# Kernel tuning notes

Hardware: AMD Instinct MI355X
Metric: run time of the kernel (lower is better)

## Reference

```python
import jax, jax.numpy as jnp
import numpy as np

S = 100000   # unique_source_num
T = 20000    # unique_target_num
N = S + T    # total nodes (sources first, then targets)
E = 1000000  # edges
SRC_DIM, EMB_DIM, TGT_DIM = 256, 128, 128


def setup_inputs() -> dict:
    key = jax.random.key(0)
    ks = jax.random.split(key, 6)
    source_feat = jax.random.normal(ks[0], (N, SRC_DIM), dtype=jnp.float32)
    src_idx = jax.random.randint(ks[1], (E,), 0, S)            # edge sources in [0, S)
    dst_idx = jax.random.randint(ks[2], (E,), 0, T)            # edge targets, target-local in [0, T)
    range_list = jax.random.randint(ks[3], (T, 2), 0, S)       # unused by the math (passed through in torch)
    # x_norm divides features; keep it bounded away from 0 like real row norms
    x_norm = jax.random.uniform(ks[4], (N,), dtype=jnp.float32, minval=0.5, maxval=1.5)
    k_e, k_w = jax.random.split(ks[5])
    embed = jax.random.normal(k_e, (SRC_DIM, EMB_DIM), dtype=jnp.float32)          # Param, std=1 init
    weight = jax.random.normal(k_w, (EMB_DIM, TGT_DIM), dtype=jnp.float32) / np.sqrt(EMB_DIM)  # is_after_relu std=1/sqrt(in)
    return {"source_feat": source_feat, "src_idx": src_idx, "dst_idx": dst_idx,
            "range_list": range_list, "x_norm": x_norm, "embed": embed, "weight": weight}


def reference(source_feat, src_idx, dst_idx, range_list, x_norm, embed, weight):
    # x = (source_feat @ embed) / x_norm[:, None]   -> [N, EMB_DIM]
    x = jnp.matmul(source_feat, embed) / x_norm[:, None]
    # message + scatter-mean aggregation onto targets (sources receive no edges,
    # so aggregating directly over the T targets == aggr_out[S:] in the torch code)
    msgs = x[src_idx]                                           # [E, EMB_DIM] gather
    summed = jax.ops.segment_sum(msgs, dst_idx, num_segments=T) # [T, EMB_DIM]
    cnt = jax.ops.segment_sum(jnp.ones((E,), dtype=x.dtype), dst_idx, num_segments=T)
    aggr = summed / jnp.maximum(cnt, 1.0)[:, None]              # mean; zero-degree -> 0
    out = jnp.matmul(aggr, weight)                              # [T, TGT_DIM]
    return out
```

## Files before the change

kernel.cpp:

```cpp
#include <hip/hip_runtime.h>
#include <cstdint>
#include <cstddef>

#define S_NUM 100000
#define T_NUM 20000
#define E_NUM 1000000

#define NB   1250
#define GT   16
#define CAP  1280
#define CH   4096
#define KB2  245
#define KB1  1563

typedef __bf16 bf16x8 __attribute__((ext_vector_type(8)));
typedef float f32x4 __attribute__((ext_vector_type(4)));

__device__ __forceinline__ unsigned short f2bf(float f) {
  unsigned int u = __float_as_uint(f);
  u += 0x7fffu + ((u >> 16) & 1u);
  return (unsigned short)(u >> 16);
}
__device__ __forceinline__ unsigned int f2bf2(float lo, float hi) {
  return (unsigned int)f2bf(lo) | ((unsigned int)f2bf(hi) << 16);
}
__device__ __forceinline__ float bflo(unsigned int v) { return __uint_as_float(v << 16); }
__device__ __forceinline__ float bfhi(unsigned int v) { return __uint_as_float(v & 0xffff0000u); }

__launch_bounds__(512)
__global__ void k12_fused(const float* __restrict__ sf, const float* __restrict__ xn,
                          const float* __restrict__ embed, unsigned short* __restrict__ xb,
                          const int* __restrict__ src_idx, const int* __restrict__ dst_idx,
                          int* __restrict__ gcursor, unsigned int* __restrict__ ebuf) {
  __shared__ __align__(16) unsigned char smem[64 * 296 * 2];
  const int tid = threadIdx.x;

  if (blockIdx.x < KB2) {
    int* bcnt  = (int*)smem;
    int* gbase = (int*)(smem + 5120);
    const int e0 = blockIdx.x * CH;
    const int e1 = (e0 + CH < E_NUM) ? (e0 + CH) : E_NUM;
    for (int i = tid; i < NB; i += 512) bcnt[i] = 0;
    __syncthreads();
    for (int e = e0 + tid; e < e1; e += 512)
      atomicAdd(&bcnt[dst_idx[e] >> 4], 1);
    __syncthreads();
    for (int i = tid; i < NB; i += 512) {
      const int cnt = bcnt[i];
      gbase[i] = (cnt > 0) ? atomicAdd(&gcursor[i], cnt) : 0;
      bcnt[i] = 0;
    }
    __syncthreads();
    for (int e = e0 + tid; e < e1; e += 512) {
      const int d = dst_idx[e];
      const int s = src_idx[e];
      const int b = d >> 4;
      const int r = atomicAdd(&bcnt[b], 1);
      const int pos = gbase[b] + r;
      if (pos < CAP)
        ebuf[(size_t)b * CAP + pos] = ((unsigned int)(d & 15) << 17) | (unsigned int)s;
    }
    return;
  }

  unsigned short (*lA)[296] = (unsigned short (*)[296])smem;
  unsigned short (*lC)[136] = (unsigned short (*)[136])smem;
  const int wave = tid >> 6;
  const int lane = tid & 63;
  const int quad = lane >> 4;
  const int l15 = lane & 15;
  const int row0 = (blockIdx.x - KB2) * 64;
  const int col0 = wave * 16;

  bf16x8 fb[8];
#pragma unroll
  for (int kc = 0; kc < 8; ++kc) {
    union { unsigned short h[8]; bf16x8 v; } u;
#pragma unroll
    for (int j = 0; j < 8; ++j)
      u.h[j] = f2bf(embed[(size_t)(kc * 32 + quad * 8 + j) * 128 + col0 + l15]);
    fb[kc] = u.v;
  }

#pragma unroll
  for (int i = 0; i < 4; ++i) {
    const int idx = i * 512 + tid;
    const int row = idx >> 5;
    const int seg = idx & 31;
    const float4* g = (const float4*)(sf + (size_t)(row0 + row) * 256 + seg * 8);
    const float4 v0 = g[0];
    const float4 v1 = g[1];
    uint4 pk;
    pk.x = f2bf2(v0.x, v0.y);
    pk.y = f2bf2(v0.z, v0.w);
    pk.z = f2bf2(v1.x, v1.y);
    pk.w = f2bf2(v1.z, v1.w);
    *(uint4*)&lA[row][seg * 8] = pk;
  }
  __syncthreads();

  f32x4 acc[4];
#pragma unroll
  for (int i = 0; i < 4; ++i) acc[i] = (f32x4){0.f, 0.f, 0.f, 0.f};

#pragma unroll
  for (int kc = 0; kc < 8; ++kc)
#pragma unroll
    for (int rt = 0; rt < 4; ++rt) {
      bf16x8 fa = *(const bf16x8*)&lA[rt * 16 + l15][kc * 32 + quad * 8];
      acc[rt] = __builtin_amdgcn_mfma_f32_16x16x32_bf16(fa, fb[kc], acc[rt], 0, 0, 0);
    }
  __syncthreads();

#pragma unroll
  for (int rt = 0; rt < 4; ++rt) {
#pragma unroll
    for (int reg = 0; reg < 4; ++reg) {
      const int row = rt * 16 + quad * 4 + reg;
      const float inv = __builtin_amdgcn_rcpf(xn[row0 + row]);
      lC[row][col0 + l15] = f2bf(acc[rt][reg] * inv);
    }
  }
  __syncthreads();

#pragma unroll
  for (int p = 0; p < 2; ++p) {
    const int i = p * 512 + tid;
    const int row = i >> 4;
    const int seg = i & 15;
    const int gr = row0 + row;
    if (gr < S_NUM)
      *(uint4*)(xb + (size_t)gr * 128 + seg * 8) = *(const uint4*)&lC[row][seg * 8];
  }
}

__launch_bounds__(512)
__global__ void k3_fused(const int* __restrict__ gcursor, const unsigned int* __restrict__ ebuf,
                         const unsigned short* __restrict__ xb,
                         const float* __restrict__ weight,
                         float* __restrict__ out) {
  __shared__ unsigned int sls[CAP];
  __shared__ int hist[GT], scn[GT], cur[GT];
  __shared__ unsigned int Pu[GT][68];
  const int b = blockIdx.x;
  const int tid = threadIdx.x;
  const int wave = tid >> 6, lane = tid & 63;
  const int quad = lane >> 4, l15 = lane & 15;

  int n = gcursor[b];
  if (n > CAP) n = CAP;
  const unsigned int* eb = ebuf + (size_t)b * CAP;

  if (tid < GT) hist[tid] = 0;
  __syncthreads();
  for (int i = tid; i < n; i += 512) atomicAdd(&hist[eb[i] >> 17], 1);
  __syncthreads();
  if (tid == 0) {
    int run = 0;
#pragma unroll
    for (int i = 0; i < GT; ++i) { scn[i] = run; run += hist[i]; }
  }
  __syncthreads();
  if (tid < GT) cur[tid] = scn[tid];
  __syncthreads();
  for (int i = tid; i < n; i += 512) {
    const unsigned int e = eb[i];
    const int r = atomicAdd(&cur[e >> 17], 1);
    sls[r] = e & 0x1FFFFu;
  }
  __syncthreads();

#pragma unroll
  for (int rep = 0; rep < 2; ++rep) {
    const int tl = wave * 2 + rep;
    const int beg = scn[tl];
    const int c = hist[tl];
    float a0 = 0.f, a1 = 0.f, b0 = 0.f, b1 = 0.f;
    int e = 0;
    for (; e + 16 <= c; e += 16) {
      int s[16];
#pragma unroll
      for (int j = 0; j < 16; ++j) s[j] = (int)sls[beg + e + j];
      unsigned int v[16];
#pragma unroll
      for (int j = 0; j < 16; ++j)
        v[j] = *(const unsigned int*)(xb + (size_t)s[j] * 128 + 2 * lane);
#pragma unroll
      for (int j = 0; j < 16; j += 2) {
        a0 += bflo(v[j]);     a1 += bfhi(v[j]);
        b0 += bflo(v[j + 1]); b1 += bfhi(v[j + 1]);
      }
    }
    for (; e + 4 <= c; e += 4) {
      int s[4];
#pragma unroll
      for (int j = 0; j < 4; ++j) s[j] = (int)sls[beg + e + j];
      unsigned int v[4];
#pragma unroll
      for (int j = 0; j < 4; ++j)
        v[j] = *(const unsigned int*)(xb + (size_t)s[j] * 128 + 2 * lane);
      a0 += bflo(v[0]); a1 += bfhi(v[0]);
      b0 += bflo(v[1]); b1 += bfhi(v[1]);
      a0 += bflo(v[2]); a1 += bfhi(v[2]);
      b0 += bflo(v[3]); b1 += bfhi(v[3]);
    }
    for (; e < c; ++e) {
      const int s0 = (int)sls[beg + e];
      const unsigned int v0 = *(const unsigned int*)(xb + (size_t)s0 * 128 + 2 * lane);
      a0 += bflo(v0); a1 += bfhi(v0);
    }
    a0 += b0; a1 += b1;
    const float inv = (c > 0) ? __builtin_amdgcn_rcpf((float)c) : 0.f;
    Pu[tl][lane] = f2bf2(a0 * inv, a1 * inv);
  }
  __syncthreads();

  const int ncol = wave * 16 + l15;
  bf16x8 wb[4];
#pragma unroll
  for (int kc = 0; kc < 4; ++kc) {
    union { unsigned short h[8]; bf16x8 v; } u;
#pragma unroll
    for (int j = 0; j < 8; ++j)
      u.h[j] = f2bf(weight[(size_t)(kc * 32 + quad * 8 + j) * 128 + ncol]);
    wb[kc] = u.v;
  }
  f32x4 o0 = (f32x4){0.f, 0.f, 0.f, 0.f};
#pragma unroll
  for (int kc = 0; kc < 4; ++kc) {
    bf16x8 p0 = *(const bf16x8*)((const unsigned short*)&Pu[l15][0] + kc * 32 + quad * 8);
    o0 = __builtin_amdgcn_mfma_f32_16x16x32_bf16(p0, wb[kc], o0, 0, 0, 0);
  }
#pragma unroll
  for (int reg = 0; reg < 4; ++reg)
    out[((size_t)b * GT + quad * 4 + reg) * 128 + ncol] = o0[reg];
}

extern "C" void kernel_launch(void* const* d_in, const int* in_sizes, int n_in,
                              void* d_out, int out_size, void* d_ws, size_t ws_size,
                              hipStream_t stream) {
  const float* sf      = (const float*)d_in[0];
  const int*   src_idx = (const int*)d_in[1];
  const int*   dst_idx = (const int*)d_in[2];
  const float* xn      = (const float*)d_in[4];
  const float* embed   = (const float*)d_in[5];
  const float* weight  = (const float*)d_in[6];
  float* out = (float*)d_out;

  char* w = (char*)d_ws;
  unsigned short* xb = (unsigned short*)(w);
  int* gcursor       = (int*)(w + 25600000);
  unsigned int* ebuf = (unsigned int*)(w + 25608192);

  hipMemsetAsync(gcursor, 0, 8192, stream);
  k12_fused<<<KB2 + KB1, 512, 0, stream>>>(sf, xn, embed, xb, src_idx, dst_idx, gcursor, ebuf);
  k3_fused<<<NB, 512, 0, stream>>>(gcursor, ebuf, xb, weight, out);
}
```

Measured before the change: 247.0 us.

## Pre-transpose weights to bf16 in prep kernel and widen gather loads

Adds a small prep kernel that zeroes the bucket cursors (replacing the memset) and writes bf16 transposed copies of embed and weight. The GEMM blocks then load their B fragments with single 16-byte vector loads instead of eight strided fp32 loads with per-element conversion. The gather loop is restructured so each half-wave handles alternate edges with 8-byte loads, and the halves are combined with a cross-lane shuffle. The cost is an extra kernel launch and a dependency on the prep kernel before the main work starts.

After: 247.1 us. Within noise of the previous version (+0.1%).

```diff
diff --git a/kernel.cpp b/kernel.cpp
--- a/kernel.cpp
+++ b/kernel.cpp
@@ -27,9 +27,27 @@
 __device__ __forceinline__ float bflo(unsigned int v) { return __uint_as_float(v << 16); }
 __device__ __forceinline__ float bfhi(unsigned int v) { return __uint_as_float(v & 0xffff0000u); }
 
+__launch_bounds__(256)
+__global__ void k0_prep(const float* __restrict__ embed, const float* __restrict__ weight,
+                        int* __restrict__ gcursor, unsigned short* __restrict__ embedT,
+                        unsigned short* __restrict__ weightT) {
+  const int idx = blockIdx.x * 256 + threadIdx.x;
+  if (idx < 2048) gcursor[idx] = 0;
+  {
+    const int col = idx & 127;
+    const int k = idx >> 7;
+    embedT[(size_t)col * 256 + k] = f2bf(embed[(size_t)k * 128 + col]);
+  }
+  if (idx < 16384) {
+    const int n = idx & 127;
+    const int k = idx >> 7;
+    weightT[(size_t)n * 128 + k] = f2bf(weight[(size_t)k * 128 + n]);
+  }
+}
+
 __launch_bounds__(512)
 __global__ void k12_fused(const float* __restrict__ sf, const float* __restrict__ xn,
-                          const float* __restrict__ embed, unsigned short* __restrict__ xb,
+                          const unsigned short* __restrict__ embedT, unsigned short* __restrict__ xb,
                           const int* __restrict__ src_idx, const int* __restrict__ dst_idx,
                           int* __restrict__ gcursor, unsigned int* __restrict__ ebuf) {
   __shared__ __align__(16) unsigned char smem[64 * 296 * 2];
@@ -72,15 +90,11 @@
   const int row0 = (blockIdx.x - KB2) * 64;
   const int col0 = wave * 16;
 
+  const unsigned short* ebT = embedT + (size_t)(col0 + l15) * 256;
   bf16x8 fb[8];
 #pragma unroll
-  for (int kc = 0; kc < 8; ++kc) {
-    union { unsigned short h[8]; bf16x8 v; } u;
-#pragma unroll
-    for (int j = 0; j < 8; ++j)
-      u.h[j] = f2bf(embed[(size_t)(kc * 32 + quad * 8 + j) * 128 + col0 + l15]);
-    fb[kc] = u.v;
-  }
+  for (int kc = 0; kc < 8; ++kc)
+    fb[kc] = *(const bf16x8*)(ebT + kc * 32 + quad * 8);
 
 #pragma unroll
   for (int i = 0; i < 4; ++i) {
@@ -137,7 +151,7 @@
 __launch_bounds__(512)
 __global__ void k3_fused(const int* __restrict__ gcursor, const unsigned int* __restrict__ ebuf,
                          const unsigned short* __restrict__ xb,
-                         const float* __restrict__ weight,
+                         const unsigned short* __restrict__ weightT,
                          float* __restrict__ out) {
   __shared__ unsigned int sls[CAP];
   __shared__ int hist[GT], scn[GT], cur[GT];
@@ -170,61 +184,57 @@
   }
   __syncthreads();
 
+  const int h = lane >> 5;
+  const int cq = lane & 31;
 #pragma unroll
   for (int rep = 0; rep < 2; ++rep) {
     const int tl = wave * 2 + rep;
     const int beg = scn[tl];
     const int c = hist[tl];
-    float a0 = 0.f, a1 = 0.f, b0 = 0.f, b1 = 0.f;
+    float t0 = 0.f, t1 = 0.f, t2 = 0.f, t3 = 0.f;
     int e = 0;
     for (; e + 16 <= c; e += 16) {
-      int s[16];
-#pragma unroll
-      for (int j = 0; j < 16; ++j) s[j] = (int)sls[beg + e + j];
-      unsigned int v[16];
-#pragma unroll
-      for (int j = 0; j < 16; ++j)
-        v[j] = *(const unsigned int*)(xb + (size_t)s[j] * 128 + 2 * lane);
-#pragma unroll
-      for (int j = 0; j < 16; j += 2) {
-        a0 += bflo(v[j]);     a1 += bfhi(v[j]);
-        b0 += bflo(v[j + 1]); b1 += bfhi(v[j + 1]);
+      int s[8];
+#pragma unroll
+      for (int j = 0; j < 8; ++j) s[j] = (int)sls[beg + e + 2 * j + h];
+      uint2 v[8];
+#pragma unroll
+      for (int j = 0; j < 8; ++j)
+        v[j] = *(const uint2*)(xb + (size_t)s[j] * 128 + 4 * cq);
+#pragma unroll
+      for (int j = 0; j < 8; ++j) {
+        t0 += bflo(v[j].x); t1 += bfhi(v[j].x);
+        t2 += bflo(v[j].y); t3 += bfhi(v[j].y);
       }
     }
-    for (; e + 4 <= c; e += 4) {
-      int s[4];
-#pragma unroll
-      for (int j = 0; j < 4; ++j) s[j] = (int)sls[beg + e + j];
-      unsigned int v[4];
-#pragma unroll
-      for (int j = 0; j < 4; ++j)
-        v[j] = *(const unsigned int*)(xb + (size_t)s[j] * 128 + 2 * lane);
-      a0 += bflo(v[0]); a1 += bfhi(v[0]);
-      b0 += bflo(v[1]); b1 += bfhi(v[1]);
-      a0 += bflo(v[2]); a1 += bfhi(v[2]);
-      b0 += bflo(v[3]); b1 += bfhi(v[3]);
-    }
-    for (; e < c; ++e) {
-      const int s0 = (int)sls[beg + e];
-      const unsigned int v0 = *(const unsigned int*)(xb + (size_t)s0 * 128 + 2 * lane);
-      a0 += bflo(v0); a1 += bfhi(v0);
-    }
-    a0 += b0; a1 += b1;
+    for (; e + 2 <= c; e += 2) {
+      const int s0 = (int)sls[beg + e + h];
+      const uint2 v0 = *(const uint2*)(xb + (size_t)s0 * 128 + 4 * cq);
+      t0 += bflo(v0.x); t1 += bfhi(v0.x);
+      t2 += bflo(v0.y); t3 += bfhi(v0.y);
+    }
+    if ((c & 1) && h == 0) {
+      const int s0 = (int)sls[beg + c - 1];
+      const uint2 v0 = *(const uint2*)(xb + (size_t)s0 * 128 + 4 * cq);
+      t0 += bflo(v0.x); t1 += bfhi(v0.x);
+      t2 += bflo(v0.y); t3 += bfhi(v0.y);
+    }
+    t0 += __shfl_xor(t0, 32, 64);
+    t1 += __shfl_xor(t1, 32, 64);
+    t2 += __shfl_xor(t2, 32, 64);
+    t3 += __shfl_xor(t3, 32, 64);
     const float inv = (c > 0) ? __builtin_amdgcn_rcpf((float)c) : 0.f;
-    Pu[tl][lane] = f2bf2(a0 * inv, a1 * inv);
+    const unsigned int pk = h ? f2bf2(t2 * inv, t3 * inv) : f2bf2(t0 * inv, t1 * inv);
+    Pu[tl][2 * cq + h] = pk;
   }
   __syncthreads();
 
   const int ncol = wave * 16 + l15;
+  const unsigned short* wT = weightT + (size_t)ncol * 128;
   bf16x8 wb[4];
 #pragma unroll
-  for (int kc = 0; kc < 4; ++kc) {
-    union { unsigned short h[8]; bf16x8 v; } u;
-#pragma unroll
-    for (int j = 0; j < 8; ++j)
-      u.h[j] = f2bf(weight[(size_t)(kc * 32 + quad * 8 + j) * 128 + ncol]);
-    wb[kc] = u.v;
-  }
+  for (int kc = 0; kc < 4; ++kc)
+    wb[kc] = *(const bf16x8*)(wT + kc * 32 + quad * 8);
   f32x4 o0 = (f32x4){0.f, 0.f, 0.f, 0.f};
 #pragma unroll
   for (int kc = 0; kc < 4; ++kc) {
@@ -248,11 +258,13 @@
   float* out = (float*)d_out;
 
   char* w = (char*)d_ws;
-  unsigned short* xb = (unsigned short*)(w);
-  int* gcursor       = (int*)(w + 25600000);
-  unsigned int* ebuf = (unsigned int*)(w + 25608192);
-
-  hipMemsetAsync(gcursor, 0, 8192, stream);
-  k12_fused<<<KB2 + KB1, 512, 0, stream>>>(sf, xn, embed, xb, src_idx, dst_idx, gcursor, ebuf);
-  k3_fused<<<NB, 512, 0, stream>>>(gcursor, ebuf, xb, weight, out);
-}
+  unsigned short* xb      = (unsigned short*)(w);
+  int* gcursor            = (int*)(w + 25600000);
+  unsigned int* ebuf      = (unsigned int*)(w + 25608192);
+  unsigned short* embedT  = (unsigned short*)(w + 32008192);
+  unsigned short* weightT = (unsigned short*)(w + 32073728);
+
+  k0_prep<<<128, 256, 0, stream>>>(embed, weight, gcursor, embedT, weightT);
+  k12_fused<<<KB2 + KB1, 512, 0, stream>>>(sf, xn, embedT, xb, src_idx, dst_idx, gcursor, ebuf);
+  k3_fused<<<NB, 512, 0, stream>>>(gcursor, ebuf, xb, weightT, out);
+}
```

## Replace global-atomic edge bucketing with per-chunk LDS sort and chunk-indexed gather

Applied to the files above, without the earlier changes.

Each edge chunk now sorts its edges by target bucket in LDS using a block-wide prefix scan. It writes the sorted chunk out contiguously, along with per-chunk bucket counts and offsets. The aggregation kernel rebuilds each bucket's edge list by scanning the per-chunk counts and binary-searching into the chunk array. This removes the global cursor atomics, the memset, and the scattered 4-byte writes into the bucket buffer. In exchange it adds strided count/base reads, an extra scan and binary search per bucket, and fragmented gather reads in the aggregation kernel.

Measured after the change: 241.1 us. 2.4% less time.

```diff
diff --git a/kernel.cpp b/kernel.cpp
--- a/kernel.cpp
+++ b/kernel.cpp
@@ -31,34 +31,74 @@
 __global__ void k12_fused(const float* __restrict__ sf, const float* __restrict__ xn,
                           const float* __restrict__ embed, unsigned short* __restrict__ xb,
                           const int* __restrict__ src_idx, const int* __restrict__ dst_idx,
-                          int* __restrict__ gcursor, unsigned int* __restrict__ ebuf) {
+                          unsigned int* __restrict__ echunk, int* __restrict__ counts,
+                          int* __restrict__ bases) {
   __shared__ __align__(16) unsigned char smem[64 * 296 * 2];
   const int tid = threadIdx.x;
 
   if (blockIdx.x < KB2) {
     int* bcnt  = (int*)smem;
-    int* gbase = (int*)(smem + 5120);
-    const int e0 = blockIdx.x * CH;
+    int* scan  = (int*)(smem + 5120);
+    int* brank = (int*)(smem + 10240);
+    unsigned int* eLDS = (unsigned int*)(smem + 15360);
+    const int c = blockIdx.x;
+    const int e0 = c * CH;
     const int e1 = (e0 + CH < E_NUM) ? (e0 + CH) : E_NUM;
-    for (int i = tid; i < NB; i += 512) bcnt[i] = 0;
-    __syncthreads();
-    for (int e = e0 + tid; e < e1; e += 512)
-      atomicAdd(&bcnt[dst_idx[e] >> 4], 1);
-    __syncthreads();
+
+    int myd[8], mys[8];
+#pragma unroll
+    for (int k = 0; k < 8; ++k) {
+      const int e = e0 + k * 512 + tid;
+      const bool ok = e < e1;
+      myd[k] = ok ? dst_idx[e] : -1;
+      mys[k] = ok ? src_idx[e] : 0;
+    }
+    for (int i = tid; i < 1280; i += 512) bcnt[i] = 0;
+    __syncthreads();
+#pragma unroll
+    for (int k = 0; k < 8; ++k)
+      if (myd[k] >= 0) atomicAdd(&bcnt[myd[k] >> 4], 1);
+    __syncthreads();
+    for (int i = tid; i < 1280; i += 512) scan[i] = bcnt[i];
+    __syncthreads();
+    for (int st = 1; st < 1280; st <<= 1) {
+      int v0 = 0, v1 = 0, v2 = 0;
+      {
+        const int j0 = tid, j1 = tid + 512, j2 = tid + 1024;
+        if (j0 >= st) v0 = scan[j0 - st];
+        if (j1 >= st) v1 = scan[j1 - st];
+        if (j2 < 1280 && j2 >= st) v2 = scan[j2 - st];
+      }
+      __syncthreads();
+      {
+        const int j0 = tid, j1 = tid + 512, j2 = tid + 1024;
+        scan[j0] += v0;
+        scan[j1] += v1;
+        if (j2 < 1280) scan[j2] += v2;
+      }
+      __syncthreads();
+    }
     for (int i = tid; i < NB; i += 512) {
       const int cnt = bcnt[i];
-      gbase[i] = (cnt > 0) ? atomicAdd(&gcursor[i], cnt) : 0;
-      bcnt[i] = 0;
-    }
-    __syncthreads();
-    for (int e = e0 + tid; e < e1; e += 512) {
-      const int d = dst_idx[e];
-      const int s = src_idx[e];
-      const int b = d >> 4;
-      const int r = atomicAdd(&bcnt[b], 1);
-      const int pos = gbase[b] + r;
-      if (pos < CAP)
-        ebuf[(size_t)b * CAP + pos] = ((unsigned int)(d & 15) << 17) | (unsigned int)s;
+      const int base = scan[i] - cnt;
+      counts[(size_t)c * NB + i] = cnt;
+      bases[(size_t)c * NB + i] = base;
+      brank[i] = base;
+    }
+    __syncthreads();
+#pragma unroll
+    for (int k = 0; k < 8; ++k)
+      if (myd[k] >= 0) {
+        const int b = myd[k] >> 4;
+        const int r = atomicAdd(&brank[b], 1);
+        eLDS[r] = ((unsigned int)(myd[k] & 15) << 17) | (unsigned int)mys[k];
+      }
+    __syncthreads();
+    {
+      uint4* dst = (uint4*)(echunk + (size_t)c * CH);
+      const uint4* src = (const uint4*)eLDS;
+      dst[tid] = src[tid];
+      dst[512 + tid] = src[512 + tid];
     }
     return;
   }
@@ -135,10 +175,13 @@
 }
 
 __launch_bounds__(512)
-__global__ void k3_fused(const int* __restrict__ gcursor, const unsigned int* __restrict__ ebuf,
+__global__ void k3_fused(const unsigned int* __restrict__ echunk, const int* __restrict__ counts,
+                         const int* __restrict__ bases,
                          const unsigned short* __restrict__ xb,
                          const float* __restrict__ weight,
                          float* __restrict__ out) {
+  __shared__ int ccnt[256], cpre[256], cbas[256];
+  __shared__ unsigned int tmp[CAP];
   __shared__ unsigned int sls[CAP];
   __shared__ int hist[GT], scn[GT], cur[GT];
   __shared__ unsigned int Pu[GT][68];
@@ -147,13 +190,39 @@
   const int wave = tid >> 6, lane = tid & 63;
   const int quad = lane >> 4, l15 = lane & 15;
 
-  int n = gcursor[b];
+  if (tid < 256) {
+    if (tid < KB2) {
+      ccnt[tid] = counts[(size_t)tid * NB + b];
+      cbas[tid] = bases[(size_t)tid * NB + b];
+    } else { ccnt[tid] = 0; cbas[tid] = 0; }
+  }
+  __syncthreads();
+  if (tid < 256) cpre[tid] = ccnt[tid];
+  __syncthreads();
+  for (int st = 1; st < 256; st <<= 1) {
+    int v = 0;
+    if (tid < 256 && tid >= st) v = cpre[tid - st];
+    __syncthreads();
+    if (tid < 256) cpre[tid] += v;
+    __syncthreads();
+  }
+  int n = cpre[255];
   if (n > CAP) n = CAP;
-  const unsigned int* eb = ebuf + (size_t)b * CAP;
+
+  for (int i = tid; i < n; i += 512) {
+    int lo = 0, hi = 255;
+    while (lo < hi) {
+      const int mid = (lo + hi) >> 1;
+      if (cpre[mid] > i) hi = mid; else lo = mid + 1;
+    }
+    const int off = i - (cpre[lo] - ccnt[lo]);
+    tmp[i] = echunk[(size_t)lo * CH + cbas[lo] + off];
+  }
+  __syncthreads();
 
   if (tid < GT) hist[tid] = 0;
   __syncthreads();
-  for (int i = tid; i < n; i += 512) atomicAdd(&hist[eb[i] >> 17], 1);
+  for (int i = tid; i < n; i += 512) atomicAdd(&hist[tmp[i] >> 17], 1);
   __syncthreads();
   if (tid == 0) {
     int run = 0;
@@ -164,7 +233,7 @@
   if (tid < GT) cur[tid] = scn[tid];
   __syncthreads();
   for (int i = tid; i < n; i += 512) {
-    const unsigned int e = eb[i];
+    const unsigned int e = tmp[i];
     const int r = atomicAdd(&cur[e >> 17], 1);
     sls[r] = e & 0x1FFFFu;
   }
@@ -248,11 +317,12 @@
   float* out = (float*)d_out;
 
   char* w = (char*)d_ws;
-  unsigned short* xb = (unsigned short*)(w);
-  int* gcursor       = (int*)(w + 25600000);
-  unsigned int* ebuf = (unsigned int*)(w + 25608192);
-
-  hipMemsetAsync(gcursor, 0, 8192, stream);
-  k12_fused<<<KB2 + KB1, 512, 0, stream>>>(sf, xn, embed, xb, src_idx, dst_idx, gcursor, ebuf);
-  k3_fused<<<NB, 512, 0, stream>>>(gcursor, ebuf, xb, weight, out);
-}
+  unsigned short* xb  = (unsigned short*)(w);
+  unsigned int* echunk = (unsigned int*)(w + 25600000);
+  int* counts          = (int*)(w + 29614080);
+  int* bases           = (int*)(w + 30839080);
+
+  k12_fused<<<KB2 + KB1, 512, 0, stream>>>(sf, xn, embed, xb, src_idx, dst_idx,
+                                           echunk, counts, bases);
+  k3_fused<<<NB, 512, 0, stream>>>(echunk, counts, bases, xb, weight, out);
+}
```
